# Kernel tuning notes

Measured on AMD Instinct MI355X. Metric: run time of the kernel, lower is better.

## Reference

```python
import jax, jax.numpy as jnp
import numpy as np

N_NODES = 100000
N_EDGES = 1600000
IN_DIM, HID, OUT = 64, 128, 128
NUM_GRAPHS = 64
BN_EPS = 1e-5


def setup_inputs() -> dict:
    key = jax.random.key(0)
    ks = jax.random.split(key, 16)
    x = jax.random.normal(ks[0], (N_NODES, IN_DIM), dtype=jnp.float32)
    edge_index = jax.random.randint(ks[1], (2, N_EDGES), 0, N_NODES, dtype=jnp.int32)
    batch = jnp.sort(jax.random.randint(ks[2], (N_NODES,), 0, NUM_GRAPHS, dtype=jnp.int32))
    dims = [IN_DIM, HID, HID, OUT]
    inp = {"x": x, "edge_index": edge_index, "batch": batch}
    for i in range(3):
        din, dout = dims[i], dims[i + 1]
        s = 1.0 / np.sqrt(din)
        inp[f"Ws{i}"] = jax.random.uniform(ks[3 + 4 * i], (din, dout), jnp.float32, -s, s)
        inp[f"Wi{i}"] = jax.random.uniform(ks[4 + 4 * i], (din, dout), jnp.float32, -s, s)
        inp[f"Wo{i}"] = jax.random.uniform(ks[5 + 4 * i], (din, dout), jnp.float32, -s, s)
        inp[f"g{i}"] = jnp.ones((dout,), jnp.float32)
        inp[f"b{i}"] = jnp.zeros((dout,), jnp.float32)
    return inp


def _dgcn(x, src, dst, Ws, Wi, Wo, gamma, beta):
    # directed aggregation: in-edges (messages from src land on dst) and out-edges
    agg_in = jax.ops.segment_sum(x[src], dst, num_segments=N_NODES)   # [N, d]
    agg_out = jax.ops.segment_sum(x[dst], src, num_segments=N_NODES)  # [N, d]
    out = x @ Ws + agg_in @ Wi + agg_out @ Wo
    out = jax.nn.relu(out)
    # BatchNorm1d (training mode, biased variance, as in torch)
    mu = out.mean(axis=0)
    var = ((out - mu) ** 2).mean(axis=0)
    return gamma * (out - mu) * jax.lax.rsqrt(var + BN_EPS) + beta


def reference(x, edge_index, batch, Ws0, Wi0, Wo0, g0, b0, Ws1, Wi1, Wo1, g1, b1,
              Ws2, Wi2, Wo2, g2, b2):
    src, dst = edge_index[0], edge_index[1]
    h = _dgcn(x, src, dst, Ws0, Wi0, Wo0, g0, b0)
    h = _dgcn(h, src, dst, Ws1, Wi1, Wo1, g1, b1)
    h = _dgcn(h, src, dst, Ws2, Wi2, Wo2, g2, b2)
    # global mean pool over graphs (dropout is identity at inference)
    sums = jax.ops.segment_sum(h, batch, num_segments=NUM_GRAPHS)       # [G, OUT]
    cnts = jax.ops.segment_sum(jnp.ones((N_NODES,), h.dtype), batch, num_segments=NUM_GRAPHS)
    return sums / jnp.maximum(cnts, 1.0)[:, None]
```

## Files before the change

### kernel.cpp

```cpp
#include <hip/hip_runtime.h>

#define NN 100000
#define NE 1600000
#define NG 64
#define BN_EPS 1e-5f

#define TOT (2 * NN)
#define STB 256

#define NB 196
#define KPB 1024
#define BDEPTH 32
#define BCAP 18432
#define EPB ((NE + 1023) / 1024)

typedef __attribute__((ext_vector_type(8))) _Float16 f16x8;
typedef __attribute__((ext_vector_type(8))) unsigned short u16x8;
typedef __attribute__((ext_vector_type(4))) float f32x4;

__device__ __forceinline__ float h2f(unsigned short u) {
  _Float16 h; __builtin_memcpy(&h, &u, 2); return (float)h;
}
__device__ __forceinline__ unsigned short f2h(float f) {
  _Float16 h = (_Float16)f; unsigned short u; __builtin_memcpy(&u, &h, 2); return u;
}

__device__ __forceinline__ int lower_bound_dev(const int* a, int n, int key) {
  int lo = 0, hi = n;
  while (lo < hi) { int mid = (lo + hi) >> 1; if (a[mid] < key) lo = mid + 1; else hi = mid; }
  return lo;
}

__global__ __launch_bounds__(256) void k_p1(const int* __restrict__ src,
    const int* __restrict__ dst, int* __restrict__ gcur, unsigned int* __restrict__ pairs) {
  __shared__ unsigned int lbuf[NB][BDEPTH];
  __shared__ int lcnt[NB], lbase[NB];
  __shared__ int sc[256];
  int t = threadIdx.x;
  if (t < NB) lcnt[t] = 0;
  __syncthreads();
  int e0 = blockIdx.x * EPB;
  int e1 = min(e0 + EPB, NE);
  for (int e = e0 + t; e < e1; e += 256) {
    int s = src[e], d = dst[e];
    {
      int key = d;
      unsigned int val = ((unsigned int)(key & (KPB - 1)) << 17) | (unsigned int)s;
      int bk = key >> 10;
      int p = atomicAdd(&lcnt[bk], 1);
      if (p < BDEPTH) lbuf[bk][p] = val;
      else { int g = atomicAdd(&gcur[bk], 1); pairs[(size_t)bk * BCAP + g] = val; }
    }
    {
      int key = s + NN;
      unsigned int val = ((unsigned int)(key & (KPB - 1)) << 17) | (unsigned int)d;
      int bk = key >> 10;
      int p = atomicAdd(&lcnt[bk], 1);
      if (p < BDEPTH) lbuf[bk][p] = val;
      else { int g = atomicAdd(&gcur[bk], 1); pairs[(size_t)bk * BCAP + g] = val; }
    }
  }
  __syncthreads();
  if (t < NB) {
    int c = min(lcnt[t], BDEPTH);
    lcnt[t] = c;
    lbase[t] = atomicAdd(&gcur[t], c);
  }
  __syncthreads();
  sc[t] = (t < NB) ? lcnt[t] : 0;
  __syncthreads();
  for (int off = 1; off < 256; off <<= 1) {
    int x = (t >= off) ? sc[t - off] : 0;
    __syncthreads();
    sc[t] += x;
    __syncthreads();
  }
  int total = sc[NB - 1];
  for (int idx = t; idx < total; idx += 256) {
    int lo = 0, hi = NB - 1;
    while (lo < hi) { int mid = (lo + hi) >> 1; if (sc[mid] > idx) hi = mid; else lo = mid + 1; }
    int within = idx - ((lo == 0) ? 0 : sc[lo - 1]);
    pairs[(size_t)lo * BCAP + lbase[lo] + within] = lbuf[lo][within];
  }
}

__global__ void k_scanNB(const int* __restrict__ gcur, int* __restrict__ fbase) {
  __shared__ int sc[256];
  int t = threadIdx.x;
  sc[t] = (t < NB) ? gcur[t] : 0;
  __syncthreads();
  for (int off = 1; off < 256; off <<= 1) {
    int x = (t >= off) ? sc[t - off] : 0;
    __syncthreads();
    sc[t] += x;
    __syncthreads();
  }
  if (t < NB) fbase[t] = (t == 0) ? 0 : sc[t - 1];
  if (t == 0) fbase[NB] = sc[NB - 1];
}

__global__ __launch_bounds__(256) void k_p2(const unsigned int* __restrict__ pairs,
    const int* __restrict__ gcur, const int* __restrict__ fbase,
    int* __restrict__ offs, int* __restrict__ nbr) {
  int b = blockIdx.x;
  int n = gcur[b];
  int base = fbase[b];
  __shared__ int hist[KPB];
  __shared__ int sc[256];
  int t = threadIdx.x;
  #pragma unroll
  for (int j = 0; j < 4; ++j) hist[t * 4 + j] = 0;
  __syncthreads();
  const unsigned int* bp = pairs + (size_t)b * BCAP;
  for (int i = t; i < n; i += 256) atomicAdd(&hist[bp[i] >> 17], 1);
  __syncthreads();
  int v[4]; int tsum = 0;
  #pragma unroll
  for (int j = 0; j < 4; ++j) { v[j] = hist[t * 4 + j]; tsum += v[j]; }
  sc[t] = tsum;
  __syncthreads();
  for (int off = 1; off < 256; off <<= 1) {
    int x = (t >= off) ? sc[t - off] : 0;
    __syncthreads();
    sc[t] += x;
    __syncthreads();
  }
  int run = (t == 0) ? 0 : sc[t - 1];
  #pragma unroll
  for (int j = 0; j < 4; ++j) {
    int key = b * KPB + t * 4 + j;
    if (key < TOT) offs[key] = base + run;
    hist[t * 4 + j] = run;
    run += v[j];
  }
  if (b == NB - 1 && t == 0) offs[TOT] = base + n;
  __syncthreads();
  for (int i = t; i < n; i += 256) {
    unsigned int u = bp[i];
    int lk = (int)(u >> 17);
    int pos = atomicAdd(&hist[lk], 1);
    nbr[base + pos] = (int)(u & 0x1FFFFu);
  }
}

__global__ __launch_bounds__(256) void k_cvt_x(const float* __restrict__ x,
                                               unsigned short* __restrict__ xb) {
  size_t i = (size_t)blockIdx.x * 256 + threadIdx.x;
  if (i >= (size_t)NN * 16) return;
  float4 v = *(const float4*)(x + i * 4);
  ushort4 o;
  o.x = f2h(v.x); o.y = f2h(v.y); o.z = f2h(v.z); o.w = f2h(v.w);
  *(ushort4*)(xb + i * 4) = o;
}

struct WtArgs { const float* W[9]; };
__global__ __launch_bounds__(256) void k_wt(WtArgs a, unsigned short* __restrict__ wt) {
  int t = blockIdx.x * 256 + threadIdx.x;
  if (t >= 15360) return;
  int p, rem, KS;
  if (t < 3072) { p = t >> 10; rem = t & 1023; KS = 2; }
  else { int u = t - 3072; p = 3 + (u >> 11); rem = u & 2047; KS = 4; }
  int ks = rem >> 9;
  int rem2 = rem & 511;
  int nt = rem2 >> 6;
  int lane = rem2 & 63;
  int L = p / 3, op = p - L * 3;
  int lbase = (L == 0) ? 0 : (24576 + (L - 1) * 49152);
  size_t dst = (size_t)lbase + (size_t)op * KS * 4096 + (size_t)(ks * 8 + nt) * 512 + lane * 8;
  const float* W = a.W[p];
  int krow = ks * 32 + (lane >> 4) * 8;
  int col = nt * 16 + (lane & 15);
  #pragma unroll
  for (int j = 0; j < 8; ++j)
    wt[dst + j] = f2h(W[(size_t)(krow + j) * 128 + col]);
}

__global__ void k_ssid(float* __restrict__ ss) {
  int t = threadIdx.x;
  ss[t] = 1.f; ss[128 + t] = 0.f;
}

template<int DIN>
__global__ __launch_bounds__(256) void k_gather(const unsigned short* __restrict__ xb,
    const float* __restrict__ ss, const int* __restrict__ offs, const int* __restrict__ nbr,
    unsigned short* __restrict__ aggi, unsigned short* __restrict__ aggo) {
  constexpr int GW = DIN / 8;
  constexpr int GPB = 256 / GW;
  int g = blockIdx.x * GPB + threadIdx.x / GW;
  if (g >= TOT) return;
  int c0 = (threadIdx.x % GW) * 8;
  int beg = offs[g], end = offs[g + 1];
  f16x8 acc;
  #pragma unroll
  for (int j = 0; j < 8; ++j) acc[j] = (_Float16)0.f;
  int k = beg;
  for (; k + 4 <= end; k += 4) {
    int n0 = nbr[k], n1 = nbr[k + 1], n2 = nbr[k + 2], n3 = nbr[k + 3];
    f16x8 v0 = *(const f16x8*)(xb + (size_t)n0 * DIN + c0);
    f16x8 v1 = *(const f16x8*)(xb + (size_t)n1 * DIN + c0);
    f16x8 v2 = *(const f16x8*)(xb + (size_t)n2 * DIN + c0);
    f16x8 v3 = *(const f16x8*)(xb + (size_t)n3 * DIN + c0);
    acc += (v0 + v1) + (v2 + v3);
  }
  for (; k < end; ++k) {
    f16x8 v = *(const f16x8*)(xb + (size_t)nbr[k] * DIN + c0);
    acc += v;
  }
  float cnt = (float)(end - beg);
  unsigned short r[8];
  #pragma unroll
  for (int j = 0; j < 8; ++j)
    r[j] = f2h(fmaf((float)acc[j], ss[c0 + j], cnt * ss[128 + c0 + j]));
  unsigned short* o = (g < NN) ? (aggi + (size_t)g * DIN) : (aggo + (size_t)(g - NN) * DIN);
  *(u16x8*)(o + c0) = *(u16x8*)r;
}

template<int KD>
__global__ __launch_bounds__(256) void k_gemm(const unsigned short* __restrict__ A0,
    const float* __restrict__ ss, const unsigned short* __restrict__ A1,
    const unsigned short* __restrict__ A2, const unsigned short* __restrict__ wt,
    unsigned short* __restrict__ out) {
  constexpr int KS = KD / 32;
  int tid = threadIdx.x;
  int lane = tid & 63;
  int w = tid >> 6;
  int m0 = blockIdx.x * 64 + w * 16;
  int arow = m0 + (lane & 15);
  int koff = (lane >> 4) * 8;
  f32x4 acc[8];
  #pragma unroll
  for (int nt = 0; nt < 8; ++nt) acc[nt] = (f32x4){0.f, 0.f, 0.f, 0.f};

  const unsigned short* As[3] = {A0, A1, A2};
  #pragma unroll
  for (int op = 0; op < 3; ++op) {
    const unsigned short* __restrict__ A = As[op];
    f16x8 af[KS];
    if (arow < NN) {
      #pragma unroll
      for (int ks = 0; ks < KS; ++ks)
        af[ks] = *(const f16x8*)(A + (size_t)arow * KD + ks * 32 + koff);
      if (op == 0) {
        #pragma unroll
        for (int ks = 0; ks < KS; ++ks) {
          #pragma unroll
          for (int j = 0; j < 8; ++j) {
            int c = ks * 32 + koff + j;
            af[ks][j] = (_Float16)fmaf((float)af[ks][j], ss[c], ss[128 + c]);
          }
        }
      }
    } else {
      #pragma unroll
      for (int ks = 0; ks < KS; ++ks)
        #pragma unroll
        for (int j = 0; j < 8; ++j) af[ks][j] = (_Float16)0.f;
    }
    #pragma unroll
    for (int ks = 0; ks < KS; ++ks) {
      #pragma unroll
      for (int nt = 0; nt < 8; ++nt) {
        f16x8 bf = *(const f16x8*)(wt + ((size_t)(op * KS + ks) * 8 + nt) * 512 + lane * 8);
        acc[nt] = __builtin_amdgcn_mfma_f32_16x16x32_f16(af[ks], bf, acc[nt], 0, 0, 0);
      }
    }
  }

  __shared__ unsigned short lds[4][16][128];
  #pragma unroll
  for (int nt = 0; nt < 8; ++nt)
    #pragma unroll
    for (int r = 0; r < 4; ++r)
      lds[w][(lane >> 4) * 4 + r][nt * 16 + (lane & 15)] = f2h(fmaxf(acc[nt][r], 0.f));
  #pragma unroll
  for (int it = 0; it < 4; ++it) {
    int rr = (lane >> 4) + it * 4;
    int cc = (lane & 15) * 8;
    int grow = m0 + rr;
    if (grow < NN)
      *(u16x8*)(out + (size_t)grow * 128 + cc) = *(const u16x8*)&lds[w][rr][cc];
  }
}

__global__ __launch_bounds__(256) void k_statsA(const unsigned short* __restrict__ hb,
                                                float* __restrict__ part) {
  int t = threadIdx.x;
  int q = t & 15;
  int gq = t >> 4;
  int c0 = q * 8;
  float s[8], s2[8];
  #pragma unroll
  for (int j = 0; j < 8; ++j) { s[j] = 0.f; s2[j] = 0.f; }
  for (int r = blockIdx.x * 16 + gq; r < NN; r += STB * 16) {
    u16x8 v = *(const u16x8*)(hb + (size_t)r * 128 + c0);
    #pragma unroll
    for (int j = 0; j < 8; ++j) {
      float f = h2f(v[j]);
      s[j] += f;
      s2[j] = fmaf(f, f, s2[j]);
    }
  }
  __shared__ float ls[256][8], ls2[256][8];
  #pragma unroll
  for (int j = 0; j < 8; ++j) { ls[t][j] = s[j]; ls2[t][j] = s2[j]; }
  __syncthreads();
  if (t < 128) {
    int qq = t >> 3, jj = t & 7;
    float S = 0.f, S2 = 0.f;
    #pragma unroll
    for (int g = 0; g < 16; ++g) {
      S += ls[g * 16 + qq][jj];
      S2 += ls2[g * 16 + qq][jj];
    }
    part[(size_t)blockIdx.x * 256 + t] = S;
    part[(size_t)blockIdx.x * 256 + 128 + t] = S2;
  }
}

__global__ __launch_bounds__(256) void k_bn_final(const float* __restrict__ part,
    const float* __restrict__ g, const float* __restrict__ b, float* __restrict__ ss) {
  int t = threadIdx.x;
  float s = 0.f;
  for (int bb = 0; bb < STB; ++bb) s += part[(size_t)bb * 256 + t];
  __shared__ float tot[256];
  tot[t] = s; __syncthreads();
  if (t < 128) {
    float mu = tot[t] / (float)NN;
    float var = tot[128 + t] / (float)NN - mu * mu;
    float rs = rsqrtf(var + BN_EPS);
    float sc = rs * g[t];
    ss[t] = sc;
    ss[128 + t] = b[t] - mu * sc;
  }
}

__global__ __launch_bounds__(128) void k_pool(const unsigned short* __restrict__ hb,
    const int* __restrict__ batch, float* __restrict__ pool) {
  int c = threadIdx.x;
  int n0 = blockIdx.x * 256;
  if (n0 >= NN) return;
  int nend = n0 + 256; if (nend > NN) nend = NN;
  int cur = batch[n0];
  float run = 0.f;
  for (int n = n0; n < nend; ++n) {
    int g = batch[n];
    if (g != cur) { atomicAdd(&pool[(size_t)cur * 128 + c], run); run = 0.f; cur = g; }
    run += h2f(hb[(size_t)n * 128 + c]);
  }
  atomicAdd(&pool[(size_t)cur * 128 + c], run);
}

__global__ __launch_bounds__(128) void k_final(const float* __restrict__ pool,
    const int* __restrict__ batch, const float* __restrict__ ss, float* __restrict__ out) {
  int g = blockIdx.x;
  int c = threadIdx.x;
  __shared__ int cnt;
  if (c == 0) {
    int lo = lower_bound_dev(batch, NN, g);
    int hi = lower_bound_dev(batch, NN, g + 1);
    cnt = hi - lo;
  }
  __syncthreads();
  float d = (float)(cnt > 1 ? cnt : 1);
  out[(size_t)g * 128 + c] = fmaf(pool[(size_t)g * 128 + c] / d, ss[c], ss[128 + c]);
}

extern "C" void kernel_launch(void* const* d_in, const int* in_sizes, int n_in,
                              void* d_out, int out_size, void* d_ws, size_t ws_size,
                              hipStream_t stream) {
  const float* x     = (const float*)d_in[0];
  const int*   ei    = (const int*)d_in[1];
  const int*   batch = (const int*)d_in[2];
  const float* gg[3] = {(const float*)d_in[6], (const float*)d_in[11], (const float*)d_in[16]};
  const float* bbv[3]= {(const float*)d_in[7], (const float*)d_in[12], (const float*)d_in[17]};
  const int* src = ei;
  const int* dst = ei + NE;

  uintptr_t p = ((uintptr_t)d_ws + 255) & ~(uintptr_t)255;
  auto alloc = [&](size_t bytes) { uintptr_t r = p; p = (p + bytes + 255) & ~(uintptr_t)255; return r; };

  unsigned int* pairs = (unsigned int*)alloc((size_t)NB * BCAP * 4);
  int* gcur  = (int*)alloc(NB * 4);
  int* fbase = (int*)alloc((NB + 1) * 4);
  int* offs  = (int*)alloc((TOT + 1) * 4);
  int* nbr   = (int*)alloc((size_t)2 * NE * 4);
  unsigned short* xb   = (unsigned short*)alloc((size_t)NN * 64 * 2);
  unsigned short* hb0  = (unsigned short*)alloc((size_t)NN * 128 * 2);
  unsigned short* hb1  = (unsigned short*)alloc((size_t)NN * 128 * 2);
  unsigned short* hb2  = (unsigned short*)alloc((size_t)NN * 128 * 2);
  unsigned short* aggi = (unsigned short*)alloc((size_t)NN * 128 * 2);
  unsigned short* aggo = (unsigned short*)alloc((size_t)NN * 128 * 2);
  unsigned short* wt   = (unsigned short*)alloc(122880 * 2);
  float* part  = (float*)alloc((size_t)STB * 256 * 4);
  float* ss_id = (float*)alloc(256 * 4);
  float* ss0   = (float*)alloc(256 * 4);
  float* ss1   = (float*)alloc(256 * 4);
  float* ss2   = (float*)alloc(256 * 4);
  float* pool  = (float*)alloc((size_t)NG * 128 * 4);

  const int gemm_grid = (NN + 63) / 64;

  hipMemsetAsync(gcur, 0, NB * sizeof(int), stream);
  k_p1<<<1024, 256, 0, stream>>>(src, dst, gcur, pairs);
  k_scanNB<<<1, 256, 0, stream>>>(gcur, fbase);
  k_p2<<<NB, 256, 0, stream>>>(pairs, gcur, fbase, offs, nbr);

  k_cvt_x<<<(NN * 16 + 255) / 256, 256, 0, stream>>>(x, xb);
  WtArgs wa;
  wa.W[0] = (const float*)d_in[3];  wa.W[1] = (const float*)d_in[4];  wa.W[2] = (const float*)d_in[5];
  wa.W[3] = (const float*)d_in[8];  wa.W[4] = (const float*)d_in[9];  wa.W[5] = (const float*)d_in[10];
  wa.W[6] = (const float*)d_in[13]; wa.W[7] = (const float*)d_in[14]; wa.W[8] = (const float*)d_in[15];
  k_wt<<<60, 256, 0, stream>>>(wa, wt);
  k_ssid<<<1, 128, 0, stream>>>(ss_id);

  k_gather<64><<<(TOT + 31) / 32, 256, 0, stream>>>(xb, ss_id, offs, nbr, aggi, aggo);
  k_gemm<64><<<gemm_grid, 256, 0, stream>>>(xb, ss_id, aggi, aggo, wt + 0, hb0);
  k_statsA<<<STB, 256, 0, stream>>>(hb0, part);
  k_bn_final<<<1, 256, 0, stream>>>(part, gg[0], bbv[0], ss0);

  k_gather<128><<<(TOT + 15) / 16, 256, 0, stream>>>(hb0, ss0, offs, nbr, aggi, aggo);
  k_gemm<128><<<gemm_grid, 256, 0, stream>>>(hb0, ss0, aggi, aggo, wt + 24576, hb1);
  k_statsA<<<STB, 256, 0, stream>>>(hb1, part);
  k_bn_final<<<1, 256, 0, stream>>>(part, gg[1], bbv[1], ss1);

  k_gather<128><<<(TOT + 15) / 16, 256, 0, stream>>>(hb1, ss1, offs, nbr, aggi, aggo);
  k_gemm<128><<<gemm_grid, 256, 0, stream>>>(hb1, ss1, aggi, aggo, wt + 73728, hb2);
  k_statsA<<<STB, 256, 0, stream>>>(hb2, part);
  k_bn_final<<<1, 256, 0, stream>>>(part, gg[2], bbv[2], ss2);

  hipMemsetAsync(pool, 0, (size_t)NG * 128 * 4, stream);
  k_pool<<<(NN + 255) / 256, 128, 0, stream>>>(hb2, batch, pool);
  k_final<<<NG, 128, 0, stream>>>(pool, batch, ss2, (float*)d_out);
}
```

Measured before the change: 589.7 us.

## Fuse BatchNorm statistics into GEMM epilogue and parallelize BN finalize

Per-channel sum and sum-of-squares are now accumulated in the GEMM epilogue from the fp32 post-ReLU values, reduced by shuffles and LDS, and written as per-block partials. This removes the separate stats pass that re-read the fp16 activations each layer. The finalize kernel now uses 128 blocks, one per channel, with a tree reduction. Smaller changes: the identity scale/shift init is folded into the weight-transpose kernel, the gather uses nontemporal stores, and the edge-bucketing constants (P1B, BDEPTH) are retuned. Statistics now come from fp32 values rather than rounded fp16, so they can differ slightly.

```diff
diff --git a/kernel.cpp b/kernel.cpp
--- a/kernel.cpp
+++ b/kernel.cpp
@@ -6,13 +6,16 @@
 #define BN_EPS 1e-5f
 
 #define TOT (2 * NN)
-#define STB 256
 
 #define NB 196
 #define KPB 1024
-#define BDEPTH 32
+#define BDEPTH 64
 #define BCAP 18432
-#define EPB ((NE + 1023) / 1024)
+#define P1B 512
+#define EPB ((NE + P1B - 1) / P1B)
+
+#define GG 1563
+#define PB 1600
 
 typedef __attribute__((ext_vector_type(8))) _Float16 f16x8;
 typedef __attribute__((ext_vector_type(8))) unsigned short u16x8;
@@ -154,9 +157,14 @@
 }
 
 struct WtArgs { const float* W[9]; };
-__global__ __launch_bounds__(256) void k_wt(WtArgs a, unsigned short* __restrict__ wt) {
+__global__ __launch_bounds__(256) void k_wt(WtArgs a, unsigned short* __restrict__ wt,
+                                            float* __restrict__ ssid) {
   int t = blockIdx.x * 256 + threadIdx.x;
-  if (t >= 15360) return;
+  if (t >= 15360) {
+    int u = t - 15360;
+    if (u < 128) { ssid[u] = 1.f; ssid[128 + u] = 0.f; }
+    return;
+  }
   int p, rem, KS;
   if (t < 3072) { p = t >> 10; rem = t & 1023; KS = 2; }
   else { int u = t - 3072; p = 3 + (u >> 11); rem = u & 2047; KS = 4; }
@@ -175,11 +183,6 @@
     wt[dst + j] = f2h(W[(size_t)(krow + j) * 128 + col]);
 }
 
-__global__ void k_ssid(float* __restrict__ ss) {
-  int t = threadIdx.x;
-  ss[t] = 1.f; ss[128 + t] = 0.f;
-}
-
 template<int DIN>
 __global__ __launch_bounds__(256) void k_gather(const unsigned short* __restrict__ xb,
     const float* __restrict__ ss, const int* __restrict__ offs, const int* __restrict__ nbr,
@@ -207,19 +210,19 @@
     acc += v;
   }
   float cnt = (float)(end - beg);
-  unsigned short r[8];
+  union { u16x8 v; unsigned short u[8]; } r;
   #pragma unroll
   for (int j = 0; j < 8; ++j)
-    r[j] = f2h(fmaf((float)acc[j], ss[c0 + j], cnt * ss[128 + c0 + j]));
+    r.u[j] = f2h(fmaf((float)acc[j], ss[c0 + j], cnt * ss[128 + c0 + j]));
   unsigned short* o = (g < NN) ? (aggi + (size_t)g * DIN) : (aggo + (size_t)(g - NN) * DIN);
-  *(u16x8*)(o + c0) = *(u16x8*)r;
+  __builtin_nontemporal_store(r.v, (u16x8*)(o + c0));
 }
 
 template<int KD>
 __global__ __launch_bounds__(256) void k_gemm(const unsigned short* __restrict__ A0,
     const float* __restrict__ ss, const unsigned short* __restrict__ A1,
     const unsigned short* __restrict__ A2, const unsigned short* __restrict__ wt,
-    unsigned short* __restrict__ out) {
+    unsigned short* __restrict__ out, float* __restrict__ part) {
   constexpr int KS = KD / 32;
   int tid = threadIdx.x;
   int lane = tid & 63;
@@ -267,11 +270,19 @@
   }
 
   __shared__ unsigned short lds[4][16][128];
+  __shared__ float sws[4][128], sws2[4][128];
+  float s8[8], s28[8];
+  #pragma unroll
+  for (int nt = 0; nt < 8; ++nt) { s8[nt] = 0.f; s28[nt] = 0.f; }
   #pragma unroll
   for (int nt = 0; nt < 8; ++nt)
     #pragma unroll
-    for (int r = 0; r < 4; ++r)
-      lds[w][(lane >> 4) * 4 + r][nt * 16 + (lane & 15)] = f2h(fmaxf(acc[nt][r], 0.f));
+    for (int r = 0; r < 4; ++r) {
+      float v = fmaxf(acc[nt][r], 0.f);
+      lds[w][(lane >> 4) * 4 + r][nt * 16 + (lane & 15)] = f2h(v);
+      s8[nt] += v;
+      s28[nt] = fmaf(v, v, s28[nt]);
+    }
   #pragma unroll
   for (int it = 0; it < 4; ++it) {
     int rr = (lane >> 4) + it * 4;
@@ -280,57 +291,51 @@
     if (grow < NN)
       *(u16x8*)(out + (size_t)grow * 128 + cc) = *(const u16x8*)&lds[w][rr][cc];
   }
-}
-
-__global__ __launch_bounds__(256) void k_statsA(const unsigned short* __restrict__ hb,
-                                                float* __restrict__ part) {
-  int t = threadIdx.x;
-  int q = t & 15;
-  int gq = t >> 4;
-  int c0 = q * 8;
-  float s[8], s2[8];
-  #pragma unroll
-  for (int j = 0; j < 8; ++j) { s[j] = 0.f; s2[j] = 0.f; }
-  for (int r = blockIdx.x * 16 + gq; r < NN; r += STB * 16) {
-    u16x8 v = *(const u16x8*)(hb + (size_t)r * 128 + c0);
+  #pragma unroll
+  for (int nt = 0; nt < 8; ++nt) {
+    s8[nt]  += __shfl_xor(s8[nt], 16);
+    s8[nt]  += __shfl_xor(s8[nt], 32);
+    s28[nt] += __shfl_xor(s28[nt], 16);
+    s28[nt] += __shfl_xor(s28[nt], 32);
+  }
+  if (lane < 16) {
     #pragma unroll
-    for (int j = 0; j < 8; ++j) {
-      float f = h2f(v[j]);
-      s[j] += f;
-      s2[j] = fmaf(f, f, s2[j]);
-    }
-  }
-  __shared__ float ls[256][8], ls2[256][8];
-  #pragma unroll
-  for (int j = 0; j < 8; ++j) { ls[t][j] = s[j]; ls2[t][j] = s2[j]; }
-  __syncthreads();
-  if (t < 128) {
-    int qq = t >> 3, jj = t & 7;
-    float S = 0.f, S2 = 0.f;
-    #pragma unroll
-    for (int g = 0; g < 16; ++g) {
-      S += ls[g * 16 + qq][jj];
-      S2 += ls2[g * 16 + qq][jj];
-    }
-    part[(size_t)blockIdx.x * 256 + t] = S;
-    part[(size_t)blockIdx.x * 256 + 128 + t] = S2;
+    for (int nt = 0; nt < 8; ++nt) {
+      sws[w][nt * 16 + lane]  = s8[nt];
+      sws2[w][nt * 16 + lane] = s28[nt];
+    }
+  }
+  __syncthreads();
+  if (tid < 128) {
+    float S  = sws[0][tid] + sws[1][tid] + sws[2][tid] + sws[3][tid];
+    float S2 = sws2[0][tid] + sws2[1][tid] + sws2[2][tid] + sws2[3][tid];
+    part[(size_t)tid * PB + blockIdx.x]         = S;
+    part[(size_t)(128 + tid) * PB + blockIdx.x] = S2;
   }
 }
 
 __global__ __launch_bounds__(256) void k_bn_final(const float* __restrict__ part,
     const float* __restrict__ g, const float* __restrict__ b, float* __restrict__ ss) {
+  int c = blockIdx.x;
   int t = threadIdx.x;
-  float s = 0.f;
-  for (int bb = 0; bb < STB; ++bb) s += part[(size_t)bb * 256 + t];
-  __shared__ float tot[256];
-  tot[t] = s; __syncthreads();
-  if (t < 128) {
-    float mu = tot[t] / (float)NN;
-    float var = tot[128 + t] / (float)NN - mu * mu;
-    float rs = rsqrtf(var + BN_EPS);
-    float sc = rs * g[t];
-    ss[t] = sc;
-    ss[128 + t] = b[t] - mu * sc;
+  float s = 0.f, s2 = 0.f;
+  for (int i = t; i < GG; i += 256) {
+    s  += part[(size_t)c * PB + i];
+    s2 += part[(size_t)(128 + c) * PB + i];
+  }
+  __shared__ float rs[256], rs2[256];
+  rs[t] = s; rs2[t] = s2; __syncthreads();
+  for (int off = 128; off > 0; off >>= 1) {
+    if (t < off) { rs[t] += rs[t + off]; rs2[t] += rs2[t + off]; }
+    __syncthreads();
+  }
+  if (t == 0) {
+    float mu = rs[0] / (float)NN;
+    float var = rs2[0] / (float)NN - mu * mu;
+    float rcp = rsqrtf(var + BN_EPS);
+    float sc = rcp * g[c];
+    ss[c] = sc;
+    ss[128 + c] = b[c] - mu * sc;
   }
 }
 
@@ -391,17 +396,15 @@
   unsigned short* aggi = (unsigned short*)alloc((size_t)NN * 128 * 2);
   unsigned short* aggo = (unsigned short*)alloc((size_t)NN * 128 * 2);
   unsigned short* wt   = (unsigned short*)alloc(122880 * 2);
-  float* part  = (float*)alloc((size_t)STB * 256 * 4);
+  float* part  = (float*)alloc((size_t)256 * PB * 4);
   float* ss_id = (float*)alloc(256 * 4);
   float* ss0   = (float*)alloc(256 * 4);
   float* ss1   = (float*)alloc(256 * 4);
   float* ss2   = (float*)alloc(256 * 4);
   float* pool  = (float*)alloc((size_t)NG * 128 * 4);
 
-  const int gemm_grid = (NN + 63) / 64;
-
   hipMemsetAsync(gcur, 0, NB * sizeof(int), stream);
-  k_p1<<<1024, 256, 0, stream>>>(src, dst, gcur, pairs);
+  k_p1<<<P1B, 256, 0, stream>>>(src, dst, gcur, pairs);
   k_scanNB<<<1, 256, 0, stream>>>(gcur, fbase);
   k_p2<<<NB, 256, 0, stream>>>(pairs, gcur, fbase, offs, nbr);
 
@@ -410,23 +413,19 @@
   wa.W[0] = (const float*)d_in[3];  wa.W[1] = (const float*)d_in[4];  wa.W[2] = (const float*)d_in[5];
   wa.W[3] = (const float*)d_in[8];  wa.W[4] = (const float*)d_in[9];  wa.W[5] = (const float*)d_in[10];
   wa.W[6] = (const float*)d_in[13]; wa.W[7] = (const float*)d_in[14]; wa.W[8] = (const float*)d_in[15];
-  k_wt<<<60, 256, 0, stream>>>(wa, wt);
-  k_ssid<<<1, 128, 0, stream>>>(ss_id);
+  k_wt<<<61, 256, 0, stream>>>(wa, wt, ss_id);
 
   k_gather<64><<<(TOT + 31) / 32, 256, 0, stream>>>(xb, ss_id, offs, nbr, aggi, aggo);
-  k_gemm<64><<<gemm_grid, 256, 0, stream>>>(xb, ss_id, aggi, aggo, wt + 0, hb0);
-  k_statsA<<<STB, 256, 0, stream>>>(hb0, part);
-  k_bn_final<<<1, 256, 0, stream>>>(part, gg[0], bbv[0], ss0);
+  k_gemm<64><<<GG, 256, 0, stream>>>(xb, ss_id, aggi, aggo, wt + 0, hb0, part);
+  k_bn_final<<<128, 256, 0, stream>>>(part, gg[0], bbv[0], ss0);
 
   k_gather<128><<<(TOT + 15) / 16, 256, 0, stream>>>(hb0, ss0, offs, nbr, aggi, aggo);
-  k_gemm<128><<<gemm_grid, 256, 0, stream>>>(hb0, ss0, aggi, aggo, wt + 24576, hb1);
-  k_statsA<<<STB, 256, 0, stream>>>(hb1, part);
-  k_bn_final<<<1, 256, 0, stream>>>(part, gg[1], bbv[1], ss1);
+  k_gemm<128><<<GG, 256, 0, stream>>>(hb0, ss0, aggi, aggo, wt + 24576, hb1, part);
+  k_bn_final<<<128, 256, 0, stream>>>(part, gg[1], bbv[1], ss1);
 
   k_gather<128><<<(TOT + 15) / 16, 256, 0, stream>>>(hb1, ss1, offs, nbr, aggi, aggo);
-  k_gemm<128><<<gemm_grid, 256, 0, stream>>>(hb1, ss1, aggi, aggo, wt + 73728, hb2);
-  k_statsA<<<STB, 256, 0, stream>>>(hb2, part);
-  k_bn_final<<<1, 256, 0, stream>>>(part, gg[2], bbv[2], ss2);
+  k_gemm<128><<<GG, 256, 0, stream>>>(hb1, ss1, aggi, aggo, wt + 73728, hb2, part);
+  k_bn_final<<<128, 256, 0, stream>>>(part, gg[2], bbv[2], ss2);
 
   hipMemsetAsync(pool, 0, (size_t)NG * 128 * 4, stream);
   k_pool<<<(NN + 255) / 256, 128, 0, stream>>>(hb2, batch, pool);
```

After: 567.1 us. -3.8%, faster.
